# Optimization experiments

Measured on AMD Instinct MI355X. Metric: run time of the kernel, lower is better.

The kernel has to match this reference:

```python
import jax, jax.numpy as jnp
import numpy as np

NUM_NET = 5
N = 10000        # nodes per net
E = 160000       # edges per net
B = 512          # molecule graphs per batch
FXD = 62         # node feature dim
FXT = 954        # cell feature dim
D = 128          # output_dim
H1 = 10          # heads in first GATConv


def setup_inputs() -> dict:
    key = jax.random.key(0)
    ks = iter(jax.random.split(key, 64))
    f32 = jnp.float32
    p = lambda shape, scale=0.05: jax.random.normal(next(ks), shape, dtype=f32) * scale
    inp = {}
    inp['x1'] = jax.random.normal(next(ks), (NUM_NET, N, FXD), dtype=f32)
    inp['ei1'] = jax.random.randint(next(ks), (NUM_NET, 2, E), 0, N, dtype=jnp.int32)
    b = ((jnp.arange(N) * B) // N).astype(jnp.int32)  # sorted, no empty graphs
    inp['batch1'] = jnp.broadcast_to(b, (NUM_NET, N))
    inp['x2'] = jax.random.normal(next(ks), (NUM_NET, N, FXD), dtype=f32)
    inp['ei2'] = jax.random.randint(next(ks), (NUM_NET, 2, E), 0, N, dtype=jnp.int32)
    inp['batch2'] = jnp.broadcast_to(b, (NUM_NET, N))
    inp['cell'] = jax.random.normal(next(ks), (B, FXT), dtype=f32)
    # per-net GAT params (stacked over NUM_NET)
    inp['W1'] = p((NUM_NET, H1 * D, FXD))
    inp['a1s'] = p((NUM_NET, H1, D)); inp['a1d'] = p((NUM_NET, H1, D))
    inp['b1'] = p((NUM_NET, H1 * D))
    inp['W2'] = p((NUM_NET, D, H1 * D))
    inp['a2s'] = p((NUM_NET, 1, D)); inp['a2d'] = p((NUM_NET, 1, D))
    inp['b2'] = p((NUM_NET, D))
    inp['Wg'] = p((NUM_NET, D, D)); inp['bg'] = p((NUM_NET, D))
    # cell reduction MLP 954->2048->512->256
    inp['Wr1'] = p((2048, FXT)); inp['br1'] = p((2048,))
    inp['Wr2'] = p((512, 2048)); inp['br2'] = p((512,))
    inp['Wr3'] = p((2 * D, 512)); inp['br3'] = p((2 * D,))
    # head MLP 512->2048->512->128->2
    inp['Wf1'] = p((2048, 4 * D)); inp['bf1'] = p((2048,))
    inp['Wf2'] = p((512, 2048)); inp['bf2'] = p((512,))
    inp['Wf3'] = p((128, 512)); inp['bf3'] = p((128,))
    inp['Wo'] = p((2, 128)); inp['bo'] = p((2,))
    return inp


def _gat(x, src, dst, W, a_s, a_d, b):
    # PyG GATConv (eval): linear -> per-head attention logits -> segment softmax over dst -> scatter-sum
    n = x.shape[0]
    H, C = a_s.shape
    h = (x @ W.T).reshape(n, H, C)
    al = (h * a_s).sum(-1)   # [n, H] source term
    ar = (h * a_d).sum(-1)   # [n, H] dest term
    e = jax.nn.leaky_relu(al[src] + ar[dst], negative_slope=0.2)  # [Ee, H]
    m = jax.ops.segment_max(e, dst, num_segments=n)               # self-loops -> no empty segments
    pe = jnp.exp(e - m[dst])
    s = jax.ops.segment_sum(pe, dst, num_segments=n)
    alpha = pe / s[dst]
    out = jax.ops.segment_sum(h[src] * alpha[:, :, None], dst, num_segments=n)
    return out.reshape(n, H * C) + b


def _branch(x, ei, batch, W1, a1s, a1d, b1, W2, a2s, a2d, b2, Wg, bg):
    n = x.shape[0]
    loops = jnp.arange(n, dtype=ei.dtype)  # add_self_loops=True in PyG GATConv
    src = jnp.concatenate([ei[0], loops])
    dst = jnp.concatenate([ei[1], loops])
    h = jax.nn.elu(_gat(x, src, dst, W1, a1s, a1d, b1))
    h = jax.nn.elu(_gat(h, src, dst, W2, a2s, a2d, b2))
    g = jax.ops.segment_max(h, batch, num_segments=B)  # global max pool
    return jax.nn.relu(g @ Wg.T + bg)


def _l2n(v):
    return v / jnp.clip(jnp.linalg.norm(v, axis=1, keepdims=True), 1e-12)


def reference(x1, ei1, batch1, x2, ei2, batch2, cell,
              W1, a1s, a1d, b1, W2, a2s, a2d, b2, Wg, bg,
              Wr1, br1, Wr2, br2, Wr3, br3,
              Wf1, bf1, Wf2, bf2, Wf3, bf3, Wo, bo):
    x11 = jnp.zeros((B, D), dtype=x1.dtype)
    x22 = jnp.zeros((B, D), dtype=x2.dtype)
    for i in range(NUM_NET):
        pr = (W1[i], a1s[i], a1d[i], b1[i], W2[i], a2s[i], a2d[i], b2[i], Wg[i], bg[i])
        x11 = x11 + _branch(x1[i], ei1[i], batch1[i], *pr) / NUM_NET
        x22 = x22 + _branch(x2[i], ei2[i], batch2[i], *pr) / NUM_NET
    c = _l2n(cell)
    c = jax.nn.relu(c @ Wr1.T + br1)
    c = jax.nn.relu(c @ Wr2.T + br2)
    c = jax.nn.relu(c @ Wr3.T + br3)
    xc = _l2n(jnp.concatenate([x11, x22, c], axis=1))
    xc = jax.nn.relu(xc @ Wf1.T + bf1)
    xc = jax.nn.relu(xc @ Wf2.T + bf2)
    xc = jax.nn.relu(xc @ Wf3.T + bf3)
    return xc @ Wo.T + bo
```

## Files before the change

### kernel.cpp

```cpp
#include <hip/hip_runtime.h>
#include <hip/hip_bf16.h>
#include <math.h>

#define NUM_NET 5
#define NN 10000
#define NE 160000
#define BB 512
#define FXD 62
#define FXT 954
#define MP 10112

typedef __bf16 bf16x8 __attribute__((ext_vector_type(8)));
typedef float f32x4 __attribute__((ext_vector_type(4)));
typedef __hip_bfloat16 bf16;

__device__ __forceinline__ float ldf(const void* p, size_t i) {
  return ((const float*)p)[i];
}
__device__ __forceinline__ float lky(float v) { return v > 0.f ? v : 0.2f * v; }
__device__ __forceinline__ float eluf(float v) { return v > 0.f ? v : (__expf(v) - 1.f); }
__device__ __forceinline__ unsigned int packbf(float a, float b) {
  __hip_bfloat162 t;
  t.x = __float2bfloat16(a);
  t.y = __float2bfloat16(b);
  return *(unsigned int*)&t;
}

struct ConvDesc {
  const void* src;
  bf16* dst;
  int M, K, Mp, Kp, mult, add, batch, pad;
};
struct ConvTable { ConvDesc d[11]; };

__global__ void convert_all_kernel(ConvTable tab) {
  ConvDesc c = tab.d[blockIdx.z];
  int b = blockIdx.y;
  if (b >= c.batch) return;
  int wave = threadIdx.x >> 6, lane = threadIdx.x & 63;
  int r = blockIdx.x * 4 + wave;
  if (r >= c.Mp) return;
  const float* srow = (const float*)c.src + ((size_t)b * c.M + r) * c.K;
  bf16* drow = c.dst + (((size_t)(b * c.mult + c.add)) * c.Mp + r) * c.Kp;
  bool rowok = r < c.M;
  for (int k = lane; k < c.Kp; k += 64) {
    float v = (rowok && k < c.K) ? srow[k] : 0.f;
    drow[k] = __float2bfloat16(v);
  }
}

__global__ void hist_kernel(const int* __restrict__ ei1, const int* __restrict__ ei2,
                            int* __restrict__ counts) {
  int z = blockIdx.z;
  int br = z & 1, net = z >> 1;
  const int* base = (br ? ei2 : ei1) + (size_t)net * 2 * NE;
  const int* dst = base + NE;
  int* cnt = counts + (size_t)z * NN;
  int i = blockIdx.x * 256 + threadIdx.x;
  if (i < NE) atomicAdd(&cnt[dst[i]], 1);
}

__global__ void scan_kernel(const int* __restrict__ counts, int* __restrict__ offs) {
  int z = blockIdx.x;
  counts += (size_t)z * NN;
  offs += (size_t)z * (NN + 1);
  __shared__ int sdata[256];
  __shared__ int s_carry;
  int t = threadIdx.x;
  if (t == 0) { s_carry = 0; offs[0] = 0; }
  __syncthreads();
  for (int base = 0; base < NN; base += 1024) {
    int loc = base + t * 4;
    int v[4];
#pragma unroll
    for (int j = 0; j < 4; j++) v[j] = (loc + j < NN) ? counts[loc + j] : 0;
    int sum4 = v[0] + v[1] + v[2] + v[3];
    sdata[t] = sum4;
    __syncthreads();
    for (int o = 1; o < 256; o <<= 1) {
      int x = (t >= o) ? sdata[t - o] : 0;
      __syncthreads();
      sdata[t] += x;
      __syncthreads();
    }
    int running = sdata[t] - sum4 + s_carry;
#pragma unroll
    for (int j = 0; j < 4; j++) {
      running += v[j];
      if (loc + j < NN) offs[loc + j + 1] = running;
    }
    int tot = sdata[255];
    __syncthreads();
    if (t == 0) s_carry += tot;
    __syncthreads();
  }
}

__global__ void scatter_kernel(const int* __restrict__ ei1, const int* __restrict__ ei2,
                               const int* __restrict__ offs, int* __restrict__ fill,
                               int* __restrict__ csrc) {
  int z = blockIdx.z;
  int br = z & 1, net = z >> 1;
  const int* base = (br ? ei2 : ei1) + (size_t)net * 2 * NE;
  const int* src = base;
  const int* dst = base + NE;
  const int* offz = offs + (size_t)z * (NN + 1);
  int* fillz = fill + (size_t)z * NN;
  int* out = csrc + (size_t)z * NE;
  int i = blockIdx.x * 256 + threadIdx.x;
  if (i < NE) {
    int d = dst[i];
    int p = offz[d] + atomicAdd(&fillz[d], 1);
    out[p] = src[i];
  }
}

__global__ __launch_bounds__(256) void walr_kernel(const void* __restrict__ W1,
                                                   const void* __restrict__ a1s,
                                                   const void* __restrict__ a1d,
                                                   bf16* __restrict__ walrb) {
  int net = blockIdx.x / 10, head = blockIdx.x % 10;
  int t = threadIdx.x, w = t >> 6, k = t & 63;
  __shared__ float ps[8][64];
  float accs = 0.f, accd = 0.f;
  for (int c = w; c < 128; c += 4) {
    float wv = (k < FXD)
        ? ldf(W1, (size_t)net * 1280 * FXD + (size_t)(head * 128 + c) * FXD + k) : 0.f;
    float vs = ldf(a1s, (size_t)net * 1280 + head * 128 + c);
    float vd = ldf(a1d, (size_t)net * 1280 + head * 128 + c);
    accs = fmaf(wv, vs, accs);
    accd = fmaf(wv, vd, accd);
  }
  ps[w][k] = accs;
  ps[4 + w][k] = accd;
  __syncthreads();
  if (w == 0) {
    float s = ps[0][k] + ps[1][k] + ps[2][k] + ps[3][k];
    float dd = ps[4][k] + ps[5][k] + ps[6][k] + ps[7][k];
    walrb[(size_t)net * 4096 + head * 64 + k] = __float2bfloat16(s);
    walrb[(size_t)net * 4096 + (16 + head) * 64 + k] = __float2bfloat16(dd);
  }
}

__global__ __launch_bounds__(256) void alpha_kernel(
    const float* __restrict__ alrA, const int* __restrict__ offsA,
    const int* __restrict__ srcsA, unsigned int* __restrict__ alphaG, int planeBase) {
  int z = blockIdx.z;
  int plane = planeBase + z;
  const float* alr = alrA + (size_t)plane * MP * 32;
  const int* offs = offsA + (size_t)plane * (NN + 1);
  const int* srcs = srcsA + (size_t)plane * NE;
  unsigned int* ag = alphaG + (size_t)z * (NE + NN) * 6;
  int wave = threadIdx.x >> 6, lane = threadIdx.x & 63;
  int d = blockIdx.x * 4 + wave;
  if (d >= NN) return;
  int e0 = offs[d], ne = offs[d + 1] - e0;
  int total = ne + 1;
  float arh[10];
#pragma unroll
  for (int h = 0; h < 10; h++) arh[h] = alr[(size_t)d * 32 + 16 + h];
  if (total <= 64) {
    int sc = (lane < ne) ? srcs[e0 + lane] : d;
    bool act = lane < total;
    const float* ap = &alr[(size_t)sc * 32];
    float v[10], m[10];
#pragma unroll
    for (int h = 0; h < 10; h++) {
      v[h] = act ? lky(ap[h] + arh[h]) : -1e30f;
      m[h] = v[h];
    }
#pragma unroll
    for (int o = 32; o > 0; o >>= 1)
#pragma unroll
      for (int h = 0; h < 10; h++) m[h] = fmaxf(m[h], __shfl_xor(m[h], o));
    float p[10], s[10];
#pragma unroll
    for (int h = 0; h < 10; h++) {
      p[h] = act ? __expf(v[h] - m[h]) : 0.f;
      s[h] = p[h];
    }
#pragma unroll
    for (int o = 32; o > 0; o >>= 1)
#pragma unroll
      for (int h = 0; h < 10; h++) s[h] += __shfl_xor(s[h], o);
    if (act) {
      float inv[10];
#pragma unroll
      for (int h = 0; h < 10; h++) inv[h] = 1.f / s[h];
      unsigned int wv[6];
#pragma unroll
      for (int hp = 0; hp < 5; hp++)
        wv[hp] = packbf(p[2 * hp] * inv[2 * hp], p[2 * hp + 1] * inv[2 * hp + 1]);
      wv[5] = (unsigned int)(d & 15);
      size_t row = (lane < ne) ? (size_t)(e0 + lane) : (size_t)(NE + d);
      unsigned int* rp = ag + row * 6;
#pragma unroll
      for (int j = 0; j < 6; j++) rp[j] = wv[j];
    }
  } else {
    float m[10], s[10];
#pragma unroll
    for (int h = 0; h < 10; h++) { m[h] = -1e30f; s[h] = 0.f; }
    for (int idx = lane; idx < total; idx += 64) {
      int sc = (idx < ne) ? srcs[e0 + idx] : d;
      const float* ap = &alr[(size_t)sc * 32];
#pragma unroll
      for (int h = 0; h < 10; h++) {
        float v = lky(ap[h] + arh[h]);
        if (v > m[h]) { s[h] = s[h] * __expf(m[h] - v) + 1.f; m[h] = v; }
        else s[h] += __expf(v - m[h]);
      }
    }
#pragma unroll
    for (int o = 32; o > 0; o >>= 1)
#pragma unroll
      for (int h = 0; h < 10; h++) {
        float mo = __shfl_xor(m[h], o), so = __shfl_xor(s[h], o);
        if (so > 0.f) {
          if (mo > m[h]) { s[h] = s[h] * __expf(m[h] - mo) + so; m[h] = mo; }
          else s[h] += so * __expf(mo - m[h]);
        }
      }
    for (int idx = lane; idx < total; idx += 64) {
      int sc = (idx < ne) ? srcs[e0 + idx] : d;
      const float* ap = &alr[(size_t)sc * 32];
      unsigned int wv[6];
#pragma unroll
      for (int hp = 0; hp < 5; hp++) {
        float v0 = lky(ap[2 * hp] + arh[2 * hp]);
        float v1 = lky(ap[2 * hp + 1] + arh[2 * hp + 1]);
        wv[hp] = packbf(__expf(v0 - m[2 * hp]) / s[2 * hp],
                        __expf(v1 - m[2 * hp + 1]) / s[2 * hp + 1]);
      }
      wv[5] = (unsigned int)(d & 15);
      size_t row = (idx < ne) ? (size_t)(e0 + idx) : (size_t)(NE + d);
      unsigned int* rp = ag + row * 6;
#pragma unroll
      for (int j = 0; j < 6; j++) rp[j] = wv[j];
    }
  }
}

struct Pref {
  uint4 xv;
  unsigned int a0, a1, a2, a3, a4;
  int dl;
  int av;
};

__device__ __forceinline__ void issue_pref(
    Pref& P, int kb, int e, int fblk, int tid, int nreal, int K_len, int e_begin,
    int d0, const int* __restrict__ srcs, const bf16* __restrict__ xp,
    const unsigned int* __restrict__ ag) {
  int ke = kb + e;
  int src;
  if (ke < nreal) {
    src = srcs[e_begin + ke];
  } else {
    int sl = ke - nreal;
    src = d0 + (sl < 16 ? sl : 0);
  }
  P.xv = *(const uint4*)&xp[(size_t)src * 64 + fblk * 8];
  P.av = 0;
  if (tid < 32 && ke < K_len) {
    P.av = 1;
    size_t row = (ke < nreal) ? (size_t)(e_begin + ke) : (size_t)(NE + d0 + (ke - nreal));
    const unsigned int* rp = ag + row * 6;
    P.a0 = rp[0]; P.a1 = rp[1]; P.a2 = rp[2]; P.a3 = rp[3]; P.a4 = rp[4];
    P.dl = (int)rp[5];
  }
}

__global__ __launch_bounds__(256) void xagg_kernel(
    const bf16* __restrict__ xpadA, const unsigned int* __restrict__ alphaG,
    const int* __restrict__ offsA, const int* __restrict__ srcsA,
    bf16* __restrict__ xagg2, int planeBase) {
  int z = blockIdx.z;
  int plane = planeBase + z;
  bf16* xagg = xagg2 + (size_t)z * 10 * MP * 64;
  int d0 = blockIdx.x * 16;
  int tid = threadIdx.x;

  if (d0 >= NN) {
    uint4 zz; zz.x = zz.y = zz.z = zz.w = 0u;
#pragma unroll
    for (int k = 0; k < 5; k++) {
      int i = tid + k * 256;
      int h = i >> 7, rem = i & 127, row = rem >> 3, seg = rem & 7;
      *(uint4*)&xagg[((size_t)h * MP + d0 + row) * 64 + seg * 8] = zz;
    }
    return;
  }

  const bf16* xp = xpadA + (size_t)plane * MP * 64;
  const int* offs = offsA + (size_t)plane * (NN + 1);
  const int* srcs = srcsA + (size_t)plane * NE;
  const unsigned int* ag = alphaG + (size_t)z * (NE + NN) * 6;

  __shared__ __align__(16) short A_s[10 * 16 * 40];
  __shared__ __align__(16) short Xt_s[64 * 40];

  int e_begin = offs[d0];
  int nreal = offs[d0 + 16] - e_begin;
  int K_len = nreal + 16;

  int e = tid & 31, fblk = tid >> 5;
  int lane = tid & 63, wave = tid >> 6;
  int l15 = lane & 15, quad = lane >> 4;
  int hbase = (wave >> 1) * 5;
  int wcol = (wave & 1) * 32;

  Pref Pn;
  issue_pref(Pn, 0, e, fblk, tid, nreal, K_len, e_begin, d0, srcs, xp, ag);

  {
    f32x4 z4 = (f32x4){0.f, 0.f, 0.f, 0.f};
    for (int i = tid; i < 800; i += 256) ((f32x4*)A_s)[i] = z4;
  }
  f32x4 acc[5][2];
#pragma unroll
  for (int i = 0; i < 5; i++)
#pragma unroll
    for (int j = 0; j < 2; j++) acc[i][j] = (f32x4){0.f, 0.f, 0.f, 0.f};
  int prev_dl = -1;
  __syncthreads();

  for (int kb = 0; kb < K_len; kb += 32) {
    Pref Pc = Pn;
    if (tid < 32) {
      if (prev_dl >= 0) {
#pragma unroll
        for (int h = 0; h < 10; h++) A_s[(h * 16 + prev_dl) * 40 + e] = 0;
      }
      prev_dl = -1;
      if (Pc.av) {
        int dlc = Pc.dl;
        A_s[(0 * 16 + dlc) * 40 + e] = (short)(Pc.a0 & 0xffff);
        A_s[(1 * 16 + dlc) * 40 + e] = (short)(Pc.a0 >> 16);
        A_s[(2 * 16 + dlc) * 40 + e] = (short)(Pc.a1 & 0xffff);
        A_s[(3 * 16 + dlc) * 40 + e] = (short)(Pc.a1 >> 16);
        A_s[(4 * 16 + dlc) * 40 + e] = (short)(Pc.a2 & 0xffff);
        A_s[(5 * 16 + dlc) * 40 + e] = (short)(Pc.a2 >> 16);
        A_s[(6 * 16 + dlc) * 40 + e] = (short)(Pc.a3 & 0xffff);
        A_s[(7 * 16 + dlc) * 40 + e] = (short)(Pc.a3 >> 16);
        A_s[(8 * 16 + dlc) * 40 + e] = (short)(Pc.a4 & 0xffff);
        A_s[(9 * 16 + dlc) * 40 + e] = (short)(Pc.a4 >> 16);
        prev_dl = dlc;
      }
    }
    {
      int fb8 = fblk * 8;
#pragma unroll
      for (int j = 0; j < 4; j++) {
        unsigned int w = ((const unsigned int*)&Pc.xv)[j];
        Xt_s[(fb8 + 2 * j) * 40 + e] = (short)(w & 0xffff);
        Xt_s[(fb8 + 2 * j + 1) * 40 + e] = (short)(w >> 16);
      }
    }
    if (kb + 32 < K_len)
      issue_pref(Pn, kb + 32, e, fblk, tid, nreal, K_len, e_begin, d0, srcs, xp, ag);
    __syncthreads();
    bf16x8 b0 = *(const bf16x8*)&Xt_s[(wcol + l15) * 40 + quad * 8];
    bf16x8 b1 = *(const bf16x8*)&Xt_s[(wcol + 16 + l15) * 40 + quad * 8];
#pragma unroll
    for (int hh = 0; hh < 5; hh++) {
      bf16x8 af = *(const bf16x8*)&A_s[((hbase + hh) * 16 + l15) * 40 + quad * 8];
      acc[hh][0] = __builtin_amdgcn_mfma_f32_16x16x32_bf16(af, b0, acc[hh][0], 0, 0, 0);
      acc[hh][1] = __builtin_amdgcn_mfma_f32_16x16x32_bf16(af, b1, acc[hh][1], 0, 0, 0);
    }
    __syncthreads();
  }

#pragma unroll
  for (int hh = 0; hh < 5; hh++) {
    int h = hbase + hh;
#pragma unroll
    for (int ft = 0; ft < 2; ft++) {
#pragma unroll
      for (int r = 0; r < 4; r++) {
        int drow = d0 + quad * 4 + r;
        xagg[((size_t)h * MP + drow) * 64 + wcol + ft * 16 + l15] =
            __float2bfloat16(acc[hh][ft][r]);
      }
    }
  }
}

__global__ __launch_bounds__(256) void fused_l1l2_kernel(
    const bf16* __restrict__ xagg2, const bf16* __restrict__ W1b,
    const void* __restrict__ b1raw, const bf16* __restrict__ W2b,
    const void* __restrict__ a2s, const void* __restrict__ a2d,
    float* __restrict__ al2A, float* __restrict__ ar2A,
    bf16* __restrict__ h2all, int planeBase) {
  int zz = blockIdx.z;
  int plane = planeBase + zz;
  int net = plane >> 1;
  long ow1 = (long)net * 1280 * 64;
  long ob1 = (long)net * 1280;
  long ow2 = (long)net * 128 * 1280;
  long oa2 = (long)net * 128;
  const bf16* xagg = xagg2 + (size_t)zz * 10 * MP * 64;
  float* al2p = al2A + (size_t)plane * NN;
  float* ar2p = ar2A + (size_t)plane * NN;
  bf16* h2 = h2all + (size_t)plane * MP * 128;
  int r0 = blockIdx.y * 64;
  __shared__ __align__(16) char uraw[52224];
  bf16* Ah = (bf16*)uraw;
  bf16* W1s = Ah + 64 * 72;
  bf16* Ps = (bf16*)uraw;
  bf16* W2s = Ps + 64 * 136;
  __shared__ float s_dot[2][2][32][2];
  int tid = threadIdx.x, lane = tid & 63, wave = tid >> 6;
  int l15 = lane & 15, quad = lane >> 4;
  int rowHalf = wave >> 1, colHalf = wave & 1;
  int wr = rowHalf * 32, wc = colHalf * 64;
  f32x4 acc2[2][4];
#pragma unroll
  for (int i = 0; i < 2; i++)
#pragma unroll
    for (int j = 0; j < 4; j++) acc2[i][j] = (f32x4){0.f, 0.f, 0.f, 0.f};

  for (int h = 0; h < 10; h++) {
    __syncthreads();
    for (int i = tid; i < 512; i += 256) {
      int r = i >> 3, seg = i & 7;
      *(uint4*)&Ah[r * 72 + seg * 8] =
          *(const uint4*)&xagg[((size_t)h * MP + r0 + r) * 64 + seg * 8];
    }
    for (int i = tid; i < 1024; i += 256) {
      int r = i >> 3, seg = i & 7;
      *(uint4*)&W1s[r * 72 + seg * 8] =
          *(const uint4*)&W1b[ow1 + (size_t)(h * 128 + r) * 64 + seg * 8];
    }
    __syncthreads();
    f32x4 acc1[4][2];
#pragma unroll
    for (int i = 0; i < 4; i++)
#pragma unroll
      for (int j = 0; j < 2; j++) acc1[i][j] = (f32x4){0.f, 0.f, 0.f, 0.f};
#pragma unroll
    for (int kc = 0; kc < 2; kc++) {
      bf16x8 af[4], bfr[2];
#pragma unroll
      for (int mi = 0; mi < 4; mi++)
        af[mi] = *(const bf16x8*)&Ah[(mi * 16 + l15) * 72 + kc * 32 + quad * 8];
#pragma unroll
      for (int ni = 0; ni < 2; ni++)
        bfr[ni] = *(const bf16x8*)&W1s[(wave * 32 + ni * 16 + l15) * 72 + kc * 32 + quad * 8];
#pragma unroll
      for (int mi = 0; mi < 4; mi++)
#pragma unroll
        for (int ni = 0; ni < 2; ni++)
          acc1[mi][ni] = __builtin_amdgcn_mfma_f32_16x16x32_bf16(af[mi], bfr[ni], acc1[mi][ni], 0, 0, 0);
    }
    __syncthreads();
#pragma unroll
    for (int ni = 0; ni < 2; ni++) {
      int pcol = wave * 32 + ni * 16 + l15;
      float bv = ldf(b1raw, ob1 + h * 128 + pcol);
#pragma unroll
      for (int mi = 0; mi < 4; mi++)
#pragma unroll
        for (int r = 0; r < 4; r++)
          Ps[(mi * 16 + quad * 4 + r) * 136 + pcol] =
              __float2bfloat16(eluf(acc1[mi][ni][r] + bv));
    }
    for (int i = tid; i < 2048; i += 256) {
      int r = i >> 4, seg = i & 15;
      *(uint4*)&W2s[r * 136 + seg * 8] =
          *(const uint4*)&W2b[ow2 + (size_t)r * 1280 + h * 128 + seg * 8];
    }
    __syncthreads();
#pragma unroll
    for (int kc = 0; kc < 4; kc++) {
      bf16x8 pa[2], pb[4];
#pragma unroll
      for (int mi = 0; mi < 2; mi++)
        pa[mi] = *(const bf16x8*)&Ps[(wr + mi * 16 + l15) * 136 + kc * 32 + quad * 8];
#pragma unroll
      for (int ni = 0; ni < 4; ni++)
        pb[ni] = *(const bf16x8*)&W2s[(wc + ni * 16 + l15) * 136 + kc * 32 + quad * 8];
#pragma unroll
      for (int mi = 0; mi < 2; mi++)
#pragma unroll
        for (int ni = 0; ni < 4; ni++)
          acc2[mi][ni] = __builtin_amdgcn_mfma_f32_16x16x32_bf16(pa[mi], pb[ni], acc2[mi][ni], 0, 0, 0);
    }
  }
  float asv[4], adv[4];
#pragma unroll
  for (int ni = 0; ni < 4; ni++) {
    int col = wc + ni * 16 + l15;
    asv[ni] = ldf(a2s, oa2 + col);
    adv[ni] = ldf(a2d, oa2 + col);
  }
#pragma unroll
  for (int mi = 0; mi < 2; mi++) {
#pragma unroll
    for (int r = 0; r < 4; r++) {
      int rl = mi * 16 + quad * 4 + r;
      int row = r0 + wr + rl;
      float psum = 0.f, pdum = 0.f;
#pragma unroll
      for (int ni = 0; ni < 4; ni++) {
        float v = acc2[mi][ni][r];
        h2[(size_t)row * 128 + wc + ni * 16 + l15] = __float2bfloat16(v);
        psum = fmaf(v, asv[ni], psum);
        pdum = fmaf(v, adv[ni], pdum);
      }
#pragma unroll
      for (int o = 1; o < 16; o <<= 1) {
        psum += __shfl_xor(psum, o);
        pdum += __shfl_xor(pdum, o);
      }
      if (l15 == 0) {
        s_dot[rowHalf][colHalf][rl][0] = psum;
        s_dot[rowHalf][colHalf][rl][1] = pdum;
      }
    }
  }
  __syncthreads();
  if (tid < 64) {
    int row = r0 + tid;
    if (row < NN) {
      int rh = tid >> 5, rl = tid & 31;
      al2p[row] = s_dot[rh][0][rl][0] + s_dot[rh][1][rl][0];
      ar2p[row] = s_dot[rh][0][rl][1] + s_dot[rh][1][rl][1];
    }
  }
}

__global__ __launch_bounds__(256) void mfma_gemm64(
    const bf16* __restrict__ A, long Az, const bf16* __restrict__ B, long Bz, int bdiv,
    const void* __restrict__ bias, long biasoff, long biaszs,
    float* __restrict__ Cf, long Cfz, int ldcf, int accum, int ncols, int brcol,
    bf16* __restrict__ Cb, long Cbz, int ldcb,
    int K, int act, float scale) {
  int z = blockIdx.z;
  int zb = bdiv ? (z >> 1) : z;
  A += (size_t)z * Az;
  B += (size_t)zb * Bz;
  if (Cf) Cf += (size_t)z * Cfz + (size_t)(z & 1) * brcol;
  if (Cb) Cb += (size_t)z * Cbz;
  const bf16* Ag = A + (size_t)blockIdx.y * 64 * K;
  const bf16* Bg = B + (size_t)blockIdx.x * 64 * K;
  __shared__ __align__(16) bf16 Asm[64 * 40];
  __shared__ __align__(16) bf16 Bsm[64 * 40];
  int tid = threadIdx.x;
  int lane = tid & 63, wave = tid >> 6;
  int wr = (wave >> 1) * 32, wc = (wave & 1) * 32;
  int l15 = lane & 15, quad = lane >> 4;
  f32x4 acc[2][2];
#pragma unroll
  for (int i = 0; i < 2; i++)
#pragma unroll
    for (int j = 0; j < 2; j++) acc[i][j] = (f32x4){0.f, 0.f, 0.f, 0.f};
  int isB = tid >> 7;
  int srow = (tid & 127) >> 1, shalf = tid & 1;
  const bf16* G = isB ? Bg : Ag;
  bf16* S = isB ? Bsm : Asm;
  for (int k0 = 0; k0 < K; k0 += 32) {
    const uint4* g = (const uint4*)(G + (size_t)srow * K + k0 + shalf * 16);
    uint4 v0 = g[0], v1 = g[1];
    __syncthreads();
    *(uint4*)&S[srow * 40 + shalf * 16] = v0;
    *(uint4*)&S[srow * 40 + shalf * 16 + 8] = v1;
    __syncthreads();
    bf16x8 af[2], bfr[2];
#pragma unroll
    for (int mi = 0; mi < 2; mi++)
      af[mi] = *(const bf16x8*)&Asm[(wr + mi * 16 + l15) * 40 + quad * 8];
#pragma unroll
    for (int ni = 0; ni < 2; ni++)
      bfr[ni] = *(const bf16x8*)&Bsm[(wc + ni * 16 + l15) * 40 + quad * 8];
#pragma unroll
    for (int mi = 0; mi < 2; mi++)
#pragma unroll
      for (int ni = 0; ni < 2; ni++)
        acc[mi][ni] = __builtin_amdgcn_mfma_f32_16x16x32_bf16(af[mi], bfr[ni], acc[mi][ni], 0, 0, 0);
  }
#pragma unroll
  for (int ni = 0; ni < 2; ni++) {
    int col = blockIdx.x * 64 + wc + ni * 16 + l15;
    if (col >= ncols) continue;
    float bv = bias ? ldf(bias, biasoff + (size_t)zb * biaszs + col) : 0.f;
#pragma unroll
    for (int mi = 0; mi < 2; mi++) {
      int rbase = blockIdx.y * 64 + wr + mi * 16 + quad * 4;
      f32x4 c = acc[mi][ni];
#pragma unroll
      for (int r = 0; r < 4; r++) {
        float v = c[r] + bv;
        if (act == 1) v = fmaxf(v, 0.f);
        else if (act == 2) v = eluf(v);
        v *= scale;
        if (Cf) {
          size_t ci = (size_t)(rbase + r) * ldcf + col;
          if (accum == 1) Cf[ci] += v;
          else if (accum == 2) atomicAdd(&Cf[ci], v);
          else Cf[ci] = v;
        }
        if (Cb) Cb[(size_t)(rbase + r) * ldcb + col] = __float2bfloat16(v);
      }
    }
  }
}

__global__ __launch_bounds__(256) void gat_agg1_kernel(
    const bf16* __restrict__ h2all, const float* __restrict__ alA, const float* __restrict__ arA,
    const int* __restrict__ offsA, const int* __restrict__ srcsA,
    const void* __restrict__ b2, bf16* __restrict__ out2all) {
  int z = blockIdx.z;
  int net = z >> 1;
  const bf16* h = h2all + (size_t)z * MP * 128;
  const float* al = alA + (size_t)z * NN;
  const float* ar = arA + (size_t)z * NN;
  const int* offs = offsA + (size_t)z * (NN + 1);
  const int* srcs = srcsA + (size_t)z * NE;
  __shared__ float2 s_pair[4][64];
  int wave = threadIdx.x >> 6, lane = threadIdx.x & 63;
  int d = blockIdx.x * 4 + wave;
  if (d >= NN) return;
  int e0 = offs[d], ne = offs[d + 1] - e0;
  int total = ne + 1;
  float ard = ar[d];
  float m, s, vcache = -1e30f;
  if (total <= 64) {
    int sc = (lane < ne) ? srcs[e0 + lane] : d;
    bool act = lane < total;
    vcache = act ? lky(al[sc] + ard) : -1e30f;
    m = vcache;
    s = act ? 1.f : 0.f;
#pragma unroll
    for (int o = 32; o > 0; o >>= 1) {
      float mo = __shfl_xor(m, o), so = __shfl_xor(s, o);
      if (so > 0.f) {
        if (mo > m) { s = s * __expf(m - mo) + so; m = mo; }
        else s += so * __expf(mo - m);
      }
    }
  } else {
    m = -1e30f; s = 0.f;
    for (int idx = lane; idx < total; idx += 64) {
      int sc = (idx < ne) ? srcs[e0 + idx] : d;
      float v = lky(al[sc] + ard);
      if (v > m) { s = s * __expf(m - v) + 1.f; m = v; }
      else s += __expf(v - m);
    }
#pragma unroll
    for (int o = 32; o > 0; o >>= 1) {
      float mo = __shfl_xor(m, o), so = __shfl_xor(s, o);
      if (so > 0.f) {
        if (mo > m) { s = s * __expf(m - mo) + so; m = mo; }
        else s += so * __expf(mo - m);
      }
    }
  }
  float inv_s = 1.f / s;
  float acc0 = 0.f, acc1v = 0.f;
  for (int c0 = 0; c0 < total; c0 += 64) {
    int idx = c0 + lane;
    int cnt = min(64, total - c0);
    if (idx < total) {
      int sc = (idx < ne) ? srcs[e0 + idx] : d;
      float v = (total <= 64) ? vcache : lky(al[sc] + ard);
      float a = __expf(v - m) * inv_s;
      s_pair[wave][lane] = make_float2(__int_as_float(sc), a);
    }
    int i = 0;
    for (; i + 2 <= cnt; i += 2) {
      float2 pA = s_pair[wave][i];
      float2 pB = s_pair[wave][i + 1];
      __hip_bfloat162 vA =
          ((const __hip_bfloat162*)(h + (size_t)__float_as_int(pA.x) * 128))[lane];
      __hip_bfloat162 vB =
          ((const __hip_bfloat162*)(h + (size_t)__float_as_int(pB.x) * 128))[lane];
      acc0 = fmaf(__bfloat162float(vA.x), pA.y, acc0);
      acc1v = fmaf(__bfloat162float(vA.y), pA.y, acc1v);
      acc0 = fmaf(__bfloat162float(vB.x), pB.y, acc0);
      acc1v = fmaf(__bfloat162float(vB.y), pB.y, acc1v);
    }
    if (i < cnt) {
      float2 pA = s_pair[wave][i];
      __hip_bfloat162 vA =
          ((const __hip_bfloat162*)(h + (size_t)__float_as_int(pA.x) * 128))[lane];
      acc0 = fmaf(__bfloat162float(vA.x), pA.y, acc0);
      acc1v = fmaf(__bfloat162float(vA.y), pA.y, acc1v);
    }
  }
  float b0 = ldf(b2, (size_t)net * 128 + 2 * lane);
  float b1v = ldf(b2, (size_t)net * 128 + 2 * lane + 1);
  __hip_bfloat162 o;
  o.x = __float2bfloat16(eluf(acc0 + b0));
  o.y = __float2bfloat16(eluf(acc1v + b1v));
  ((__hip_bfloat162*)(out2all + ((size_t)z * NN + d) * 128))[lane] = o;
}

__global__ __launch_bounds__(256) void pool_max_kernel(const bf16* __restrict__ out2all,
                                                       bf16* __restrict__ gall) {
  int z = blockIdx.z;
  const bf16* h = out2all + (size_t)z * NN * 128;
  bf16* g = gall + (size_t)z * BB * 128;
  int wave = threadIdx.x >> 6, lane = threadIdx.x & 63;
  int b = blockIdx.x * 4 + wave;
  if (b >= BB) return;
  int n0 = (b * NN + BB - 1) / BB;
  int n1 = ((b + 1) * NN + BB - 1) / BB;
  if (n1 > NN) n1 = NN;
  float mx = -1e30f, my = -1e30f;
  for (int n = n0; n < n1; n++) {
    __hip_bfloat162 v = ((const __hip_bfloat162*)(h + (size_t)n * 128))[lane];
    mx = fmaxf(mx, __bfloat162float(v.x));
    my = fmaxf(my, __bfloat162float(v.y));
  }
  __hip_bfloat162 o;
  o.x = __float2bfloat16(mx);
  o.y = __float2bfloat16(my);
  ((__hip_bfloat162*)(g + (size_t)b * 128))[lane] = o;
}

__global__ __launch_bounds__(256) void l2norm_b_kernel(const float* __restrict__ x,
                                                       bf16* __restrict__ y, int Din, int Kp) {
  int r = blockIdx.x, t = threadIdx.x;
  __shared__ float red[256];
  float s = 0.f;
  for (int i = t; i < Din; i += 256) {
    float v = x[(size_t)r * Din + i];
    s += v * v;
  }
  red[t] = s;
  __syncthreads();
  for (int o = 128; o > 0; o >>= 1) { if (t < o) red[t] += red[t + o]; __syncthreads(); }
  float inv = 1.f / fmaxf(sqrtf(red[0]), 1e-12f);
  for (int i = t; i < Kp; i += 256) {
    float v = (i < Din) ? x[(size_t)r * Din + i] : 0.f;
    y[(size_t)r * Kp + i] = __float2bfloat16(v * inv);
  }
}

__global__ void final_out_kernel(const float* __restrict__ f3, const void* __restrict__ Wo,
                                 const void* __restrict__ bo, float* __restrict__ out) {
  int r = blockIdx.x;
  int lane = threadIdx.x;
  float x0 = f3[(size_t)r * 128 + lane], x1v = f3[(size_t)r * 128 + 64 + lane];
  float s0 = x0 * ldf(Wo, lane) + x1v * ldf(Wo, 64 + lane);
  float s1 = x0 * ldf(Wo, 128 + lane) + x1v * ldf(Wo, 192 + lane);
#pragma unroll
  for (int o = 32; o > 0; o >>= 1) { s0 += __shfl_down(s0, o); s1 += __shfl_down(s1, o); }
  if (lane == 0) {
    out[r * 2] = s0 + ldf(bo, 0);
    out[r * 2 + 1] = s1 + ldf(bo, 1);
  }
}


extern "C" void kernel_launch(void* const* d_in, const int* in_sizes, int n_in,
                              void* d_out, int out_size, void* d_ws, size_t ws_size,
                              hipStream_t stream) {
  const void* x1 = d_in[0];
  const int* ei1 = (const int*)d_in[1];
  const void* x2 = d_in[3];
  const int* ei2 = (const int*)d_in[4];
  const void* cell = d_in[6];
  const void* W1 = d_in[7];
  const void* a1s = d_in[8];
  const void* a1d = d_in[9];
  const void* b1 = d_in[10];
  const void* W2 = d_in[11];
  const void* a2s = d_in[12];
  const void* a2d = d_in[13];
  const void* b2 = d_in[14];
  const void* Wg = d_in[15];
  const void* bg = d_in[16];
  const void* Wr1 = d_in[17]; const void* br1 = d_in[18];
  const void* Wr2 = d_in[19]; const void* br2 = d_in[20];
  const void* Wr3 = d_in[21]; const void* br3 = d_in[22];
  const void* Wf1 = d_in[23]; const void* bf1 = d_in[24];
  const void* Wf2 = d_in[25]; const void* bf2 = d_in[26];
  const void* Wf3 = d_in[27]; const void* bf3 = d_in[28];
  const void* Wo = d_in[29]; const void* bo = d_in[30];

  char* base = (char*)d_ws;
  size_t off = 0;
  auto alloc = [&](size_t bytes) -> void* {
    void* p = base + off;
    off = (off + bytes + 255) & ~(size_t)255;
    return p;
  };
  bf16* d_xpad = (bf16*)alloc((size_t)10 * MP * 64 * 2);
  bf16* d_W1b = (bf16*)alloc((size_t)5 * 1280 * 64 * 2);
  bf16* d_W2b = (bf16*)alloc((size_t)5 * 128 * 1280 * 2);
  bf16* d_Wgb = (bf16*)alloc((size_t)5 * 128 * 128 * 2);
  bf16* d_Wr1b = (bf16*)alloc((size_t)2048 * 960 * 2);
  bf16* d_Wr2b = (bf16*)alloc((size_t)512 * 2048 * 2);
  bf16* d_Wr3b = (bf16*)alloc((size_t)256 * 512 * 2);
  bf16* d_Wf1b = (bf16*)alloc((size_t)2048 * 512 * 2);
  bf16* d_Wf2b = (bf16*)alloc((size_t)512 * 2048 * 2);
  bf16* d_Wf3b = (bf16*)alloc((size_t)128 * 512 * 2);
  int* d_offs = (int*)alloc((size_t)10 * (NN + 1) * 4);
  int* d_srcs = (int*)alloc((size_t)10 * NE * 4);
  int* d_cnt = (int*)alloc((size_t)10 * NN * 4);
  bf16* d_walrb = (bf16*)alloc((size_t)5 * 64 * 64 * 2);
  float* d_alr = (float*)alloc((size_t)10 * MP * 32 * 4);
  float* d_al2 = (float*)alloc((size_t)20 * NN * 4);
  float* d_ar2 = d_al2 + (size_t)10 * NN;
  bf16* d_h2all = (bf16*)alloc((size_t)10 * MP * 128 * 2);
  unsigned int* d_alphaG = (unsigned int*)alloc((size_t)10 * (NE + NN) * 24);
  char* uni = base + off;
  size_t avail = (ws_size > off) ? (ws_size - off) : 0;
  size_t need10 = (size_t)10 * 10 * MP * 64 * 2;
  int G = (avail >= need10 + 65536) ? 10 : 5;
  bf16* d_xagg2 = (bf16*)uni;
  bf16* d_out2all = (bf16*)uni;
  bf16* d_gall = (bf16*)(uni + 25600000);
  float* d_xc = (float*)(uni + 26910720);
  bf16* d_xcb = (bf16*)(uni + 27959296);
  bf16* d_cnb = (bf16*)(uni + 28483584);
  bf16* d_m1b = (bf16*)(uni + 29466624);
  bf16* d_m2b = (bf16*)(uni + 31563776);
  float* d_f3 = (float*)(uni + 32088064);

  ConvTable tab;
  tab.d[0] = {x1, d_xpad, NN, FXD, MP, 64, 2, 0, 5, 0};
  tab.d[1] = {x2, d_xpad, NN, FXD, MP, 64, 2, 1, 5, 0};
  tab.d[2] = {W1, d_W1b, 1280, FXD, 1280, 64, 1, 0, 5, 0};
  tab.d[3] = {W2, d_W2b, 128, 1280, 128, 1280, 1, 0, 5, 0};
  tab.d[4] = {Wg, d_Wgb, 128, 128, 128, 128, 1, 0, 5, 0};
  tab.d[5] = {Wr1, d_Wr1b, 2048, FXT, 2048, 960, 1, 0, 1, 0};
  tab.d[6] = {Wr2, d_Wr2b, 512, 2048, 512, 2048, 1, 0, 1, 0};
  tab.d[7] = {Wr3, d_Wr3b, 256, 512, 256, 512, 1, 0, 1, 0};
  tab.d[8] = {Wf1, d_Wf1b, 2048, 512, 2048, 512, 1, 0, 1, 0};
  tab.d[9] = {Wf2, d_Wf2b, 512, 2048, 512, 2048, 1, 0, 1, 0};
  tab.d[10] = {Wf3, d_Wf3b, 128, 512, 128, 512, 1, 0, 1, 0};
  convert_all_kernel<<<dim3((MP + 3) / 4, 5, 11), 256, 0, stream>>>(tab);

  hipMemsetAsync(d_cnt, 0, (size_t)10 * NN * 4, stream);
  hist_kernel<<<dim3((NE + 255) / 256, 1, 10), 256, 0, stream>>>(ei1, ei2, d_cnt);
  scan_kernel<<<10, 256, 0, stream>>>(d_cnt, d_offs);
  hipMemsetAsync(d_cnt, 0, (size_t)10 * NN * 4, stream);
  scatter_kernel<<<dim3((NE + 255) / 256, 1, 10), 256, 0, stream>>>(ei1, ei2, d_offs, d_cnt, d_srcs);

  walr_kernel<<<50, 256, 0, stream>>>(W1, a1s, a1d, d_walrb);
  mfma_gemm64<<<dim3(1, MP / 64, 10), 256, 0, stream>>>(
      d_xpad, (long)MP * 64, d_walrb, 4096, 1, nullptr, 0, 0,
      d_alr, (long)MP * 32, 32, 0, 32, 0, nullptr, 0, 0, 64, 0, 1.f);

  for (int pb = 0; pb < 10; pb += G) {
    alpha_kernel<<<dim3(NN / 4, 1, G), 256, 0, stream>>>(d_alr, d_offs, d_srcs, d_alphaG, pb);
    xagg_kernel<<<dim3(MP / 16, 1, G), 256, 0, stream>>>(d_xpad, d_alphaG, d_offs, d_srcs, d_xagg2, pb);
    fused_l1l2_kernel<<<dim3(1, MP / 64, G), 256, 0, stream>>>(
        d_xagg2, d_W1b, b1, d_W2b, a2s, a2d, d_al2, d_ar2, d_h2all, pb);
  }

  hipMemsetAsync(d_xc, 0, (size_t)BB * 512 * 4, stream);
  gat_agg1_kernel<<<dim3(2500, 1, 10), 256, 0, stream>>>(
      d_h2all, d_al2, d_ar2, d_offs, d_srcs, b2, d_out2all);
  pool_max_kernel<<<dim3(BB / 4, 1, 10), 256, 0, stream>>>(d_out2all, d_gall);
  mfma_gemm64<<<dim3(2, BB / 64, 10), 256, 0, stream>>>(
      d_gall, (long)BB * 128, d_Wgb, 128 * 128, 1,
      bg, 0, 128,
      d_xc, 0, 512, 2, 128, 128, nullptr, 0, 0, 128, 1, 0.2f);

  l2norm_b_kernel<<<BB, 256, 0, stream>>>((const float*)cell, d_cnb, FXT, 960);
  mfma_gemm64<<<dim3(32, 8, 1), 256, 0, stream>>>(
      d_cnb, 0, d_Wr1b, 0, 0, br1, 0, 0, nullptr, 0, 0, 0, 1 << 30, 0, d_m1b, 0, 2048, 960, 1, 1.f);
  mfma_gemm64<<<dim3(8, 8, 1), 256, 0, stream>>>(
      d_m1b, 0, d_Wr2b, 0, 0, br2, 0, 0, nullptr, 0, 0, 0, 1 << 30, 0, d_m2b, 0, 512, 2048, 1, 1.f);
  mfma_gemm64<<<dim3(4, 8, 1), 256, 0, stream>>>(
      d_m2b, 0, d_Wr3b, 0, 0, br3, 0, 0, d_xc + 256, 0, 512, 0, 1 << 30, 0, nullptr, 0, 0, 512, 1, 1.f);

  l2norm_b_kernel<<<BB, 256, 0, stream>>>(d_xc, d_xcb, 512, 512);
  mfma_gemm64<<<dim3(32, 8, 1), 256, 0, stream>>>(
      d_xcb, 0, d_Wf1b, 0, 0, bf1, 0, 0, nullptr, 0, 0, 0, 1 << 30, 0, d_m1b, 0, 2048, 512, 1, 1.f);
  mfma_gemm64<<<dim3(8, 8, 1), 256, 0, stream>>>(
      d_m1b, 0, d_Wf2b, 0, 0, bf2, 0, 0, nullptr, 0, 0, 0, 1 << 30, 0, d_m2b, 0, 512, 2048, 1, 1.f);
  mfma_gemm64<<<dim3(2, 8, 1), 256, 0, stream>>>(
      d_m2b, 0, d_Wf3b, 0, 0, bf3, 0, 0, d_f3, 0, 128, 0, 1 << 30, 0, nullptr, 0, 0, 512, 1, 1.f);
  final_out_kernel<<<BB, 64, 0, stream>>>(d_f3, Wo, bo, (float*)d_out);
}
```

Before: 963.6 us.

## Compact convert launch grid and halve W2 shared tile in fused GAT kernel

```diff
diff --git a/kernel.cpp b/kernel.cpp
--- a/kernel.cpp
+++ b/kernel.cpp
@@ -29,16 +29,21 @@
 struct ConvDesc {
   const void* src;
   bf16* dst;
-  int M, K, Mp, Kp, mult, add, batch, pad;
+  int M, K, Mp, Kp, mult, add, batch, rowBlocks;
 };
-struct ConvTable { ConvDesc d[11]; };
+struct ConvTable { ConvDesc d[11]; int blk0[12]; };
 
 __global__ void convert_all_kernel(ConvTable tab) {
-  ConvDesc c = tab.d[blockIdx.z];
-  int b = blockIdx.y;
-  if (b >= c.batch) return;
+  int bid = blockIdx.x;
+  int di = 0;
+#pragma unroll
+  for (int d = 1; d < 11; d++) di += (bid >= tab.blk0[d]);
+  ConvDesc c = tab.d[di];
+  int local = bid - tab.blk0[di];
+  int b = local / c.rowBlocks;
+  int rb = local - b * c.rowBlocks;
   int wave = threadIdx.x >> 6, lane = threadIdx.x & 63;
-  int r = blockIdx.x * 4 + wave;
+  int r = rb * 4 + wave;
   if (r >= c.Mp) return;
   const float* srow = (const float*)c.src + ((size_t)b * c.M + r) * c.K;
   bf16* drow = c.dst + (((size_t)(b * c.mult + c.add)) * c.Mp + r) * c.Kp;
@@ -404,7 +409,7 @@
   float* ar2p = ar2A + (size_t)plane * NN;
   bf16* h2 = h2all + (size_t)plane * MP * 128;
   int r0 = blockIdx.y * 64;
-  __shared__ __align__(16) char uraw[52224];
+  __shared__ __align__(16) char uraw[35840];
   bf16* Ah = (bf16*)uraw;
   bf16* W1s = Ah + 64 * 72;
   bf16* Ps = (bf16*)uraw;
@@ -465,26 +470,38 @@
           Ps[(mi * 16 + quad * 4 + r) * 136 + pcol] =
               __float2bfloat16(eluf(acc1[mi][ni][r] + bv));
     }
-    for (int i = tid; i < 2048; i += 256) {
-      int r = i >> 4, seg = i & 15;
-      *(uint4*)&W2s[r * 136 + seg * 8] =
+    for (int i = tid; i < 1024; i += 256) {
+      int r = i >> 3, seg = i & 7;
+      *(uint4*)&W2s[r * 72 + seg * 8] =
           *(const uint4*)&W2b[ow2 + (size_t)r * 1280 + h * 128 + seg * 8];
     }
     __syncthreads();
 #pragma unroll
-    for (int kc = 0; kc < 4; kc++) {
-      bf16x8 pa[2], pb[4];
-#pragma unroll
-      for (int mi = 0; mi < 2; mi++)
-        pa[mi] = *(const bf16x8*)&Ps[(wr + mi * 16 + l15) * 136 + kc * 32 + quad * 8];
-#pragma unroll
-      for (int ni = 0; ni < 4; ni++)
-        pb[ni] = *(const bf16x8*)&W2s[(wc + ni * 16 + l15) * 136 + kc * 32 + quad * 8];
-#pragma unroll
-      for (int mi = 0; mi < 2; mi++)
+    for (int kh = 0; kh < 2; kh++) {
+      if (kh) {
+        __syncthreads();
+        for (int i = tid; i < 1024; i += 256) {
+          int r = i >> 3, seg = i & 7;
+          *(uint4*)&W2s[r * 72 + seg * 8] =
+              *(const uint4*)&W2b[ow2 + (size_t)r * 1280 + h * 128 + 64 + seg * 8];
+        }
+        __syncthreads();
+      }
+#pragma unroll
+      for (int kc = 0; kc < 2; kc++) {
+        bf16x8 pa[2], pb[4];
+#pragma unroll
+        for (int mi = 0; mi < 2; mi++)
+          pa[mi] = *(const bf16x8*)&Ps[(wr + mi * 16 + l15) * 136 + kh * 64 + kc * 32 + quad * 8];
 #pragma unroll
         for (int ni = 0; ni < 4; ni++)
-          acc2[mi][ni] = __builtin_amdgcn_mfma_f32_16x16x32_bf16(pa[mi], pb[ni], acc2[mi][ni], 0, 0, 0);
+          pb[ni] = *(const bf16x8*)&W2s[(wc + ni * 16 + l15) * 72 + kc * 32 + quad * 8];
+#pragma unroll
+        for (int mi = 0; mi < 2; mi++)
+#pragma unroll
+          for (int ni = 0; ni < 4; ni++)
+            acc2[mi][ni] = __builtin_amdgcn_mfma_f32_16x16x32_bf16(pa[mi], pb[ni], acc2[mi][ni], 0, 0, 0);
+      }
     }
   }
   float asv[4], adv[4];
@@ -821,18 +838,26 @@
   float* d_f3 = (float*)(uni + 32088064);
 
   ConvTable tab;
-  tab.d[0] = {x1, d_xpad, NN, FXD, MP, 64, 2, 0, 5, 0};
-  tab.d[1] = {x2, d_xpad, NN, FXD, MP, 64, 2, 1, 5, 0};
-  tab.d[2] = {W1, d_W1b, 1280, FXD, 1280, 64, 1, 0, 5, 0};
-  tab.d[3] = {W2, d_W2b, 128, 1280, 128, 1280, 1, 0, 5, 0};
-  tab.d[4] = {Wg, d_Wgb, 128, 128, 128, 128, 1, 0, 5, 0};
-  tab.d[5] = {Wr1, d_Wr1b, 2048, FXT, 2048, 960, 1, 0, 1, 0};
-  tab.d[6] = {Wr2, d_Wr2b, 512, 2048, 512, 2048, 1, 0, 1, 0};
-  tab.d[7] = {Wr3, d_Wr3b, 256, 512, 256, 512, 1, 0, 1, 0};
-  tab.d[8] = {Wf1, d_Wf1b, 2048, 512, 2048, 512, 1, 0, 1, 0};
-  tab.d[9] = {Wf2, d_Wf2b, 512, 2048, 512, 2048, 1, 0, 1, 0};
-  tab.d[10] = {Wf3, d_Wf3b, 128, 512, 128, 512, 1, 0, 1, 0};
-  convert_all_kernel<<<dim3((MP + 3) / 4, 5, 11), 256, 0, stream>>>(tab);
+  tab.d[0] = {x1, d_xpad, NN, FXD, MP, 64, 2, 0, 5, (MP + 3) / 4};
+  tab.d[1] = {x2, d_xpad, NN, FXD, MP, 64, 2, 1, 5, (MP + 3) / 4};
+  tab.d[2] = {W1, d_W1b, 1280, FXD, 1280, 64, 1, 0, 5, 320};
+  tab.d[3] = {W2, d_W2b, 128, 1280, 128, 1280, 1, 0, 5, 32};
+  tab.d[4] = {Wg, d_Wgb, 128, 128, 128, 128, 1, 0, 5, 32};
+  tab.d[5] = {Wr1, d_Wr1b, 2048, FXT, 2048, 960, 1, 0, 1, 512};
+  tab.d[6] = {Wr2, d_Wr2b, 512, 2048, 512, 2048, 1, 0, 1, 128};
+  tab.d[7] = {Wr3, d_Wr3b, 256, 512, 256, 512, 1, 0, 1, 64};
+  tab.d[8] = {Wf1, d_Wf1b, 2048, 512, 2048, 512, 1, 0, 1, 512};
+  tab.d[9] = {Wf2, d_Wf2b, 512, 2048, 512, 2048, 1, 0, 1, 128};
+  tab.d[10] = {Wf3, d_Wf3b, 128, 512, 128, 512, 1, 0, 1, 32};
+  {
+    int cum = 0;
+    tab.blk0[0] = 0;
+    for (int i = 0; i < 11; i++) {
+      cum += tab.d[i].rowBlocks * tab.d[i].batch;
+      tab.blk0[i + 1] = cum;
+    }
+    convert_all_kernel<<<dim3(cum), 256, 0, stream>>>(tab);
+  }
 
   hipMemsetAsync(d_cnt, 0, (size_t)10 * NN * 4, stream);
   hist_kernel<<<dim3((NE + 255) / 256, 1, 10), 256, 0, stream>>>(ei1, ei2, d_cnt);
```

New measurement: 995.7 us. 1.03x slower.
